# Performance work log

Measured on AMD Instinct MI355X. Metric: run time of the kernel, lower is better.

## Reference

```python
import jax, jax.numpy as jnp
import numpy as np

N_NODES = 100000
N_EDGES = 1600000
F_IN = 128
HID = 128
N_CLS = 10
BN_EPS = 1e-5


def setup_inputs() -> dict:
    key = jax.random.key(0)
    ks = jax.random.split(key, 20)
    d = {}
    d['x'] = jax.random.normal(ks[0], (N_NODES, F_IN), dtype=jnp.float32)
    d['edge_index'] = jax.random.randint(ks[1], (2, N_EDGES), 0, N_NODES, dtype=jnp.int64)
    d['edge_weights'] = jax.random.uniform(ks[2], (N_EDGES,), dtype=jnp.float32)
    s1 = 1.0 / np.sqrt(F_IN)
    s2 = 1.0 / np.sqrt(HID)
    d['W1'] = jax.random.normal(ks[3], (F_IN, HID), dtype=jnp.float32) * s1
    d['b1'] = jax.random.normal(ks[4], (HID,), dtype=jnp.float32) * 0.01
    d['g1'] = jax.random.uniform(ks[5], (HID,), dtype=jnp.float32) + 0.5
    d['be1'] = jax.random.normal(ks[6], (HID,), dtype=jnp.float32) * 0.01
    d['W2'] = jax.random.normal(ks[7], (HID, HID), dtype=jnp.float32) * s2
    d['b2'] = jax.random.normal(ks[8], (HID,), dtype=jnp.float32) * 0.01
    d['g2'] = jax.random.uniform(ks[9], (HID,), dtype=jnp.float32) + 0.5
    d['be2'] = jax.random.normal(ks[10], (HID,), dtype=jnp.float32) * 0.01
    d['W3'] = jax.random.normal(ks[11], (HID, HID), dtype=jnp.float32) * s2
    d['b3'] = jax.random.normal(ks[12], (HID,), dtype=jnp.float32) * 0.01
    d['g3'] = jax.random.uniform(ks[13], (HID,), dtype=jnp.float32) + 0.5
    d['be3'] = jax.random.normal(ks[14], (HID,), dtype=jnp.float32) * 0.01
    d['Wlin'] = jax.random.normal(ks[15], (3 * HID, N_CLS), dtype=jnp.float32) / np.sqrt(3 * HID)
    d['blin'] = jax.random.normal(ks[16], (N_CLS,), dtype=jnp.float32) * 0.01
    return d


def _gcn_norm(edge_index, edge_weights, n):
    # add self loops with weight 1 (PyG gcn_norm default fill_value=1)
    loops = jnp.arange(n, dtype=edge_index.dtype)
    row = jnp.concatenate([edge_index[0], loops])   # source j
    col = jnp.concatenate([edge_index[1], loops])   # target i
    ew = jnp.concatenate([edge_weights, jnp.ones((n,), edge_weights.dtype)])
    deg = jax.ops.segment_sum(ew, col, num_segments=n)  # in-degree by weight
    dis = jnp.where(deg > 0, jax.lax.rsqrt(deg), 0.0)
    norm = dis[row] * ew * dis[col]                     # [E+N]
    return row, col, norm


def _gcn_conv(x, row, col, norm, W, b, n):
    h = x @ W                                            # [N, H]
    msg = h[row] * norm[:, None]                         # gather + scale
    out = jax.ops.segment_sum(msg, col, num_segments=n)  # scatter-add
    return out + b


def _bn_relu(x, g, be):
    # BatchNorm with track_running_stats=False: batch stats, biased variance
    mean = jnp.mean(x, axis=0)
    var = jnp.mean((x - mean) ** 2, axis=0)
    y = (x - mean) * jax.lax.rsqrt(var + BN_EPS) * g + be
    return jax.nn.relu(y)


def reference(x, edge_index, edge_weights, W1, b1, g1, be1, W2, b2, g2, be2,
              W3, b3, g3, be3, Wlin, blin):
    n = x.shape[0]
    row, col, norm = _gcn_norm(edge_index, edge_weights, n)
    o1 = _bn_relu(_gcn_conv(x, row, col, norm, W1, b1, n), g1, be1)
    o2 = _bn_relu(_gcn_conv(o1, row, col, norm, W2, b2, n), g2, be2)
    o3 = _bn_relu(_gcn_conv(o2, row, col, norm, W3, b3, n), g3, be3)
    emb = jnp.concatenate([o1, o2, o3], axis=1)          # [N, 3H]
    return emb @ Wlin + blin                             # [N, C]
```

## Files before the change

kernel.cpp:

```cpp
#include <hip/hip_runtime.h>

#define BN_EPS 1e-5f
#define AGG_GRID 2048
#define RED1 64
#define NB 512
#define CAP 4864
#define BIN_KE 16

typedef __attribute__((ext_vector_type(8))) short short8;
typedef __attribute__((ext_vector_type(4))) float f32x4;

static __device__ __forceinline__ float4 ld4(const float* p){ return *reinterpret_cast<const float4*>(p); }
static __device__ __forceinline__ void st4(float* p, float4 v){ *reinterpret_cast<float4*>(p) = v; }
static __device__ __forceinline__ unsigned short f2bf(float f){
  unsigned u = __float_as_uint(f);
  u += 0x7fffu + ((u>>16)&1u);
  return (unsigned short)(u>>16);
}
static __device__ __forceinline__ void fma_bf4(float4& a, float s, uint2 w){
  float v0 = __uint_as_float(w.x << 16);
  float v1 = __uint_as_float(w.x & 0xffff0000u);
  float v2 = __uint_as_float(w.y << 16);
  float v3 = __uint_as_float(w.y & 0xffff0000u);
  a.x = fmaf(s,v0,a.x); a.y = fmaf(s,v1,a.y); a.z = fmaf(s,v2,a.z); a.w = fmaf(s,v3,a.w);
}
static __device__ __forceinline__ float4 unpack_bf4(uint2 w){
  return make_float4(__uint_as_float(w.x << 16), __uint_as_float(w.x & 0xffff0000u),
                     __uint_as_float(w.y << 16), __uint_as_float(w.y & 0xffff0000u));
}
static __device__ __forceinline__ uint2 pack_bf4(float4 v){
  uint2 pk;
  pk.x = (unsigned)f2bf(v.x) | ((unsigned)f2bf(v.y)<<16);
  pk.y = (unsigned)f2bf(v.z) | ((unsigned)f2bf(v.w)<<16);
  return pk;
}

__global__ __launch_bounds__(256) void k_zero(int* p, int n){
  int i = blockIdx.x*256 + threadIdx.x;
  if (i < n) p[i] = 0;
}

__global__ __launch_bounds__(256) void k_prepW(const float* __restrict__ W, unsigned short* __restrict__ Wt){
  int idx = blockIdx.x*256 + threadIdx.x;
  int k = idx >> 7, n = idx & 127;
  Wt[n*128 + k] = f2bf(W[idx]);
}

__global__ __launch_bounds__(256) void k_prepWlin(const float* __restrict__ Wlin, unsigned short* __restrict__ WlinT){
  int idx = blockIdx.x*256 + threadIdx.x;
  if (idx >= 6144) return;
  int l = idx >> 11, rem = idx & 2047;
  int n = rem >> 7, k = rem & 127;
  float v = (n < 10) ? Wlin[((size_t)l*128 + k)*10 + n] : 0.f;
  WlinT[(size_t)l*2048 + n*128 + k] = f2bf(v);
}

__global__ __launch_bounds__(256) void k_bin(const int* __restrict__ row, const int* __restrict__ col,
                                             const float* __restrict__ ew, int* __restrict__ bucketCnt,
                                             int2* __restrict__ bin, int E){
  __shared__ int hist[NB];
  int t = threadIdx.x;
  hist[t] = 0; hist[t+256] = 0;
  __syncthreads();
  int base0 = blockIdx.x*(256*BIN_KE) + t;
  int rank[BIN_KE];
  #pragma unroll
  for (int j=0;j<BIN_KE;++j){
    int e = base0 + j*256;
    if (e < E) rank[j] = atomicAdd(&hist[col[e]>>8], 1);
  }
  __syncthreads();
  int c0 = hist[t], c1 = hist[t+256];
  __syncthreads();
  if (c0) hist[t]     = atomicAdd(&bucketCnt[t],     c0);
  if (c1) hist[t+256] = atomicAdd(&bucketCnt[t+256], c1);
  __syncthreads();
  #pragma unroll
  for (int j=0;j<BIN_KE;++j){
    int e = base0 + j*256;
    if (e < E){
      int d = col[e];
      int bk = d >> 8;
      int pos = hist[bk] + rank[j];
      if (pos < CAP)
        bin[(size_t)bk*CAP + pos] = make_int2(row[e] | ((d & 255) << 17), __float_as_int(ew[e]));
    }
  }
}

__global__ void k_scan512(const int* __restrict__ cnt, int* __restrict__ start){
  __shared__ int sh[NB];
  int t = threadIdx.x;
  int c = cnt[t]; if (c > CAP) c = CAP;
  sh[t] = c;
  __syncthreads();
  for (int off=1; off<NB; off<<=1){
    int x = (t>=off) ? sh[t-off] : 0;
    __syncthreads();
    sh[t] += x;
    __syncthreads();
  }
  start[t] = sh[t] - c;
}

__global__ __launch_bounds__(256) void k_csr(const int2* __restrict__ bin, const int* __restrict__ bucketCnt,
                                             const int* __restrict__ bucketStart, int2* __restrict__ csr,
                                             int* __restrict__ rstart, float* __restrict__ deg, int N){
  __shared__ int hist[256], scn[256];
  __shared__ float degl[256];
  int b = blockIdx.x, t = threadIdx.x;
  hist[t] = 0; degl[t] = 0.f;
  __syncthreads();
  int m = bucketCnt[b]; if (m > CAP) m = CAP;
  const int2* bb = bin + (size_t)b*CAP;
  for (int i = t; i < m; i += 256){
    int2 r = bb[i];
    int dl = (r.x >> 17) & 255;
    atomicAdd(&hist[dl], 1);
    atomicAdd(&degl[dl], __int_as_float(r.y));
  }
  __syncthreads();
  int c = hist[t];
  scn[t] = c;
  __syncthreads();
  for (int off=1; off<256; off<<=1){
    int x = (t>=off) ? scn[t-off] : 0;
    __syncthreads();
    scn[t] += x;
    __syncthreads();
  }
  int base = bucketStart[b];
  int g = (b<<8) + t;
  if (g < N){
    rstart[g] = base + scn[t] - c;
    deg[g] = 1.f + degl[t];
    if (g == N-1) rstart[N] = base + scn[t];
  }
  __syncthreads();
  hist[t] = scn[t] - c;
  __syncthreads();
  for (int i = t; i < m; i += 256){
    int2 r = bb[i];
    int dl = (r.x >> 17) & 255;
    int pos = atomicAdd(&hist[dl], 1);
    csr[base + pos] = make_int2(r.x & 0x1FFFF, r.y);
  }
}

__global__ __launch_bounds__(256) void k_dis(const float* __restrict__ deg, float* __restrict__ dis, int N){
  int i = blockIdx.x*256 + threadIdx.x;
  if (i < N) dis[i] = rsqrtf(deg[i]);
}

__global__ __launch_bounds__(256) void k_norm(int2* __restrict__ csr, const float* __restrict__ dis, int M){
  int e = blockIdx.x*256 + threadIdx.x;
  if (e < M){
    int2 r = csr[e];
    r.y = __float_as_int(__int_as_float(r.y) * dis[r.x]);
    csr[e] = r;
  }
}

template<bool BN, bool LIN, bool LININIT>
__global__ __launch_bounds__(256) void k_gemm_mfma(const void* __restrict__ Ap, const unsigned short* __restrict__ Wt,
                                                   const float* __restrict__ abv, unsigned short* __restrict__ h,
                                                   const unsigned short* __restrict__ WlinT,
                                                   const float* __restrict__ blin, float* __restrict__ out, int N){
  __shared__ unsigned short Al[64*136];
  __shared__ unsigned short Wl[128*136];
  int t = threadIdx.x;
  int row0 = blockIdx.x*64;
  #pragma unroll
  for (int i=0;i<8;++i){
    int idx = t + 256*i;
    int r = idx>>5, cg = idx&31;
    float4 v;
    if (!BN){
      v = make_float4(0.f,0.f,0.f,0.f);
      if (row0 + r < N) v = ld4((const float*)Ap + ((size_t)(row0+r)<<7) + cg*4);
    } else {
      uint2 raw = make_uint2(0u,0u);
      if (row0 + r < N) raw = *reinterpret_cast<const uint2*>((const unsigned short*)Ap + ((size_t)(row0+r)<<7) + cg*4);
      v = unpack_bf4(raw);
      float4 av = ld4(abv + cg*4), cv = ld4(abv + 128 + cg*4);
      v.x = fmaxf(fmaf(v.x,av.x,cv.x),0.f);
      v.y = fmaxf(fmaf(v.y,av.y,cv.y),0.f);
      v.z = fmaxf(fmaf(v.z,av.z,cv.z),0.f);
      v.w = fmaxf(fmaf(v.w,av.w,cv.w),0.f);
    }
    *reinterpret_cast<uint2*>(&Al[r*136 + cg*4]) = pack_bf4(v);
  }
  #pragma unroll
  for (int i=0;i<8;++i){
    int idx = t + 256*i;
    int n = idx>>4, c8 = idx&15;
    *reinterpret_cast<uint4*>(&Wl[n*136 + c8*8]) =
      *reinterpret_cast<const uint4*>(&Wt[n*128 + c8*8]);
  }

  int w = t>>6, lane = t&63, quad = lane>>4, lr = lane&15;
  short8 bl[4];
  if (LIN){
    #pragma unroll
    for (int q4=0;q4<4;++q4)
      bl[q4] = *reinterpret_cast<const short8*>(&WlinT[lr*128 + q4*32 + quad*8]);
  }
  __syncthreads();

  f32x4 acc[8];
  #pragma unroll
  for (int j=0;j<8;++j) acc[j] = (f32x4){0.f,0.f,0.f,0.f};
  f32x4 accL = (f32x4){0.f,0.f,0.f,0.f};
  #pragma unroll
  for (int kk=0; kk<128; kk+=32){
    short8 a = *reinterpret_cast<const short8*>(&Al[(w*16+lr)*136 + kk + quad*8]);
    #pragma unroll
    for (int j=0;j<8;++j){
      short8 b = *reinterpret_cast<const short8*>(&Wl[(j*16+lr)*136 + kk + quad*8]);
      acc[j] = __builtin_amdgcn_mfma_f32_16x16x32_bf16(a, b, acc[j], 0, 0, 0);
    }
    if (LIN) accL = __builtin_amdgcn_mfma_f32_16x16x32_bf16(a, bl[kk>>5], accL, 0, 0, 0);
  }
  if (LIN && lr < 10){
    #pragma unroll
    for (int r=0;r<4;++r){
      int rr = row0 + w*16 + quad*4 + r;
      if (rr < N){
        if (LININIT) out[(size_t)rr*10 + lr] = blin[lr] + accL[r];
        else         out[(size_t)rr*10 + lr] += accL[r];
      }
    }
  }
  __syncthreads();
  #pragma unroll
  for (int j=0;j<8;++j)
    #pragma unroll
    for (int r=0;r<4;++r)
      Al[(w*16 + quad*4 + r)*136 + j*16 + lr] = f2bf(acc[j][r]);
  __syncthreads();
  #pragma unroll
  for (int i=0;i<8;++i){
    int idx = t + 256*i;
    int r = idx>>5, cg = idx&31;
    if (row0 + r < N)
      *reinterpret_cast<uint2*>(&h[((size_t)(row0+r)<<7) + cg*4]) =
        *reinterpret_cast<const uint2*>(&Al[r*136 + cg*4]);
  }
}

__global__ __launch_bounds__(256) void k_agg(const unsigned short* __restrict__ h, const int2* __restrict__ csr,
                                             const int* __restrict__ rstart, const float* __restrict__ dis,
                                             const float* __restrict__ bias, unsigned short* __restrict__ o,
                                             float* __restrict__ partials, int N){
  __shared__ float ls[256];
  int t = threadIdx.x;
  ls[t] = 0.f;
  __syncthreads();
  int lane = t & 31, gy = t >> 5;
  float4 bv = ld4(bias + lane*4);
  float4 ssum = make_float4(0.f,0.f,0.f,0.f);
  float4 ssq  = make_float4(0.f,0.f,0.f,0.f);
  for (int g = blockIdx.x*8 + gy; g < N; g += AGG_GRID*8){
    int s = rstart[g], n = rstart[g+1] - s;
    float dg = dis[g];
    float4 acc = make_float4(0.f,0.f,0.f,0.f);
    fma_bf4(acc, dg*dg, *reinterpret_cast<const uint2*>(h + ((size_t)g<<7) + lane*4));
    int i = 0;
    for (; i+3 < n; i += 4){
      int2 e0 = csr[s+i], e1 = csr[s+i+1], e2 = csr[s+i+2], e3 = csr[s+i+3];
      uint2 r0 = *reinterpret_cast<const uint2*>(h + ((size_t)e0.x<<7) + lane*4);
      uint2 r1 = *reinterpret_cast<const uint2*>(h + ((size_t)e1.x<<7) + lane*4);
      uint2 r2 = *reinterpret_cast<const uint2*>(h + ((size_t)e2.x<<7) + lane*4);
      uint2 r3 = *reinterpret_cast<const uint2*>(h + ((size_t)e3.x<<7) + lane*4);
      fma_bf4(acc, __int_as_float(e0.y)*dg, r0);
      fma_bf4(acc, __int_as_float(e1.y)*dg, r1);
      fma_bf4(acc, __int_as_float(e2.y)*dg, r2);
      fma_bf4(acc, __int_as_float(e3.y)*dg, r3);
    }
    for (; i < n; ++i){
      int2 e0 = csr[s+i];
      fma_bf4(acc, __int_as_float(e0.y)*dg, *reinterpret_cast<const uint2*>(h + ((size_t)e0.x<<7) + lane*4));
    }
    acc.x += bv.x; acc.y += bv.y; acc.z += bv.z; acc.w += bv.w;
    *reinterpret_cast<uint2*>(o + ((size_t)g<<7) + lane*4) = pack_bf4(acc);
    ssum.x += acc.x; ssum.y += acc.y; ssum.z += acc.z; ssum.w += acc.w;
    ssq.x = fmaf(acc.x,acc.x,ssq.x); ssq.y = fmaf(acc.y,acc.y,ssq.y);
    ssq.z = fmaf(acc.z,acc.z,ssq.z); ssq.w = fmaf(acc.w,acc.w,ssq.w);
  }
  int f = lane*4;
  atomicAdd(&ls[f+0], ssum.x); atomicAdd(&ls[f+1], ssum.y);
  atomicAdd(&ls[f+2], ssum.z); atomicAdd(&ls[f+3], ssum.w);
  atomicAdd(&ls[128+f+0], ssq.x); atomicAdd(&ls[128+f+1], ssq.y);
  atomicAdd(&ls[128+f+2], ssq.z); atomicAdd(&ls[128+f+3], ssq.w);
  __syncthreads();
  partials[(size_t)blockIdx.x*256 + t] = ls[t];
}

__global__ __launch_bounds__(256) void k_bn_red1(const float* __restrict__ partials, float* __restrict__ out1){
  int t = threadIdx.x, b = blockIdx.x;
  int rows = AGG_GRID / RED1;
  const float* p = partials + (size_t)b*rows*256;
  float s0 = 0.f, s1 = 0.f, s2 = 0.f, s3 = 0.f;
  for (int i=0;i<rows;i+=4){
    s0 += p[(size_t)(i+0)*256 + t];
    s1 += p[(size_t)(i+1)*256 + t];
    s2 += p[(size_t)(i+2)*256 + t];
    s3 += p[(size_t)(i+3)*256 + t];
  }
  out1[(size_t)b*256 + t] = (s0+s1)+(s2+s3);
}

__global__ void k_bn_fin(const float* __restrict__ out1, const float* __restrict__ gam,
                         const float* __restrict__ bet, float* __restrict__ ab, int N){
  __shared__ float sh[256];
  int t = threadIdx.x;
  float s = 0.f;
  #pragma unroll 4
  for (int i=0;i<RED1;++i) s += out1[(size_t)i*256 + t];
  sh[t] = s;
  __syncthreads();
  if (t < 128){
    float invN = 1.f/(float)N;
    float mean = sh[t]*invN;
    float var = fmaxf(sh[128+t]*invN - mean*mean, 0.f);
    float a = gam[t]*rsqrtf(var + BN_EPS);
    ab[t] = a;
    ab[128+t] = bet[t] - mean*a;
  }
}

__global__ __launch_bounds__(256) void k_lin(const unsigned short* __restrict__ o, const float* __restrict__ Wl_g,
                                             const float* __restrict__ ab, float* __restrict__ out, int N){
  __shared__ float Wl[1280];
  __shared__ float abL[256];
  int t = threadIdx.x;
  for (int i=t;i<1280;i+=256) Wl[i] = Wl_g[i];
  abL[t] = ab[t];
  __syncthreads();
  int row = blockIdx.x*256 + t;
  if (row >= N) return;
  float acc[10];
  #pragma unroll
  for (int c=0;c<10;++c) acc[c] = out[(size_t)row*10 + c];
  const unsigned short* orow = o + ((size_t)row<<7);
  #pragma unroll 4
  for (int k=0;k<128;k+=4){
    float4 v = unpack_bf4(*reinterpret_cast<const uint2*>(orow + k));
    float4 av = ld4(abL + k), cv = ld4(abL + 128 + k);
    v.x = fmaxf(fmaf(v.x,av.x,cv.x),0.f);
    v.y = fmaxf(fmaf(v.y,av.y,cv.y),0.f);
    v.z = fmaxf(fmaf(v.z,av.z,cv.z),0.f);
    v.w = fmaxf(fmaf(v.w,av.w,cv.w),0.f);
    #pragma unroll
    for (int c=0;c<10;++c){
      acc[c] = fmaf(v.x, Wl[(k+0)*10+c], acc[c]);
      acc[c] = fmaf(v.y, Wl[(k+1)*10+c], acc[c]);
      acc[c] = fmaf(v.z, Wl[(k+2)*10+c], acc[c]);
      acc[c] = fmaf(v.w, Wl[(k+3)*10+c], acc[c]);
    }
  }
  #pragma unroll
  for (int c=0;c<10;++c) out[(size_t)row*10 + c] = acc[c];
}


extern "C" void kernel_launch(void* const* d_in, const int* in_sizes, int n_in,
                              void* d_out, int out_size, void* d_ws, size_t ws_size,
                              hipStream_t stream){
  const float* x    = (const float*)d_in[0];
  const int*   ei   = (const int*)d_in[1];
  const float* ew   = (const float*)d_in[2];
  const float* W[3]  = {(const float*)d_in[3], (const float*)d_in[7],  (const float*)d_in[11]};
  const float* b[3]  = {(const float*)d_in[4], (const float*)d_in[8],  (const float*)d_in[12]};
  const float* g[3]  = {(const float*)d_in[5], (const float*)d_in[9],  (const float*)d_in[13]};
  const float* be[3] = {(const float*)d_in[6], (const float*)d_in[10], (const float*)d_in[14]};
  const float* Wlin = (const float*)d_in[15];
  const float* blin = (const float*)d_in[16];
  float* out = (float*)d_out;

  int N = in_sizes[0] / 128;
  int E = in_sizes[2];
  const int* row = ei;
  const int* col = ei + E;

  char* p = (char*)d_ws;
  auto carve = [&](size_t bytes) -> void* {
    void* q = (void*)p;
    p += (bytes + 255) & ~(size_t)255;
    return q;
  };
  int*   bucketCnt   = (int*)  carve((size_t)NB*4);
  int*   bucketStart = (int*)  carve((size_t)NB*4);
  float* deg      = (float*)carve((size_t)N*4);
  float* dis      = (float*)carve((size_t)N*4);
  int*   rstart   = (int*)  carve((size_t)(N+1)*4);
  float* partials = (float*)carve((size_t)AGG_GRID*256*4);
  float* red1     = (float*)carve((size_t)RED1*256*4);
  float* ab       = (float*)carve(3*256*4);
  unsigned short* Wt    = (unsigned short*)carve((size_t)3*128*128*2);
  unsigned short* WlinT = (unsigned short*)carve((size_t)3*16*128*2);
  unsigned short* h  = (unsigned short*)carve((size_t)N*128*2);
  unsigned short* o  = (unsigned short*)carve((size_t)N*128*2);
  int2*  csr      = (int2*) carve((size_t)E*8);
  int2*  bin      = (int2*) carve((size_t)NB*CAP*8);

  int gN = (N+255)/256, gE = (E+255)/256;
  int gBin = (E + 256*BIN_KE - 1) / (256*BIN_KE);

  k_zero<<<2,256,0,stream>>>(bucketCnt, NB);
  for (int l=0;l<3;++l)
    k_prepW<<<64,256,0,stream>>>(W[l], Wt + (size_t)l*128*128);
  k_prepWlin<<<24,256,0,stream>>>(Wlin, WlinT);
  k_bin    <<<gBin,256,0,stream>>>(row, col, ew, bucketCnt, bin, E);
  k_scan512<<<1,NB,0,stream>>>(bucketCnt, bucketStart);
  k_csr    <<<NB,256,0,stream>>>(bin, bucketCnt, bucketStart, csr, rstart, deg, N);
  k_dis    <<<gN,256,0,stream>>>(deg, dis, N);
  k_norm   <<<gE,256,0,stream>>>(csr, dis, E);

  int gGemm = (N+63)/64;
  k_gemm_mfma<false,false,false><<<gGemm,256,0,stream>>>(x, Wt, nullptr, h, nullptr, nullptr, nullptr, N);
  k_agg    <<<AGG_GRID,256,0,stream>>>(h, csr, rstart, dis, b[0], o, partials, N);
  k_bn_red1<<<RED1,256,0,stream>>>(partials, red1);
  k_bn_fin <<<1,256,0,stream>>>(red1, g[0], be[0], ab, N);
  k_gemm_mfma<true,true,true><<<gGemm,256,0,stream>>>(o, Wt + 128*128, ab, h, WlinT, blin, out, N);
  k_agg    <<<AGG_GRID,256,0,stream>>>(h, csr, rstart, dis, b[1], o, partials, N);
  k_bn_red1<<<RED1,256,0,stream>>>(partials, red1);
  k_bn_fin <<<1,256,0,stream>>>(red1, g[1], be[1], ab + 256, N);
  k_gemm_mfma<true,true,false><<<gGemm,256,0,stream>>>(o, Wt + 2*128*128, ab + 256, h, WlinT + 2048, blin, out, N);
  k_agg    <<<AGG_GRID,256,0,stream>>>(h, csr, rstart, dis, b[2], o, partials, N);
  k_bn_red1<<<RED1,256,0,stream>>>(partials, red1);
  k_bn_fin <<<1,256,0,stream>>>(red1, g[2], be[2], ab + 512, N);
  k_lin    <<<gN,256,0,stream>>>(o, Wlin + (size_t)2*1280, ab + 512, out, N);
}
```

Before: 515.5 us.

## Fold source-degree scaling into GEMM epilogue and fuse BN reduction into aggregation

The source-side D^-1/2 factor moves out of the per-edge weights and into the GEMM epilogue, which scales each h row by dis[row]. The target-side factor is applied once per node at the end of aggregation. This removes the k_norm and k_dis passes over edges and nodes. The BatchNorm statistics reduction is folded into k_agg with a last-block-done atomic counter, replacing two extra kernels per layer, and the weight prep and zeroing kernels are merged into one launch. In exchange, a single block serially reduces all 2048 partials, and h is now stored in bf16 after scaling by dis, which slightly changes rounding.

```diff
diff --git a/kernel.cpp b/kernel.cpp
--- a/kernel.cpp
+++ b/kernel.cpp
@@ -2,7 +2,6 @@
 
 #define BN_EPS 1e-5f
 #define AGG_GRID 2048
-#define RED1 64
 #define NB 512
 #define CAP 4864
 #define BIN_KE 16
@@ -11,7 +10,6 @@
 typedef __attribute__((ext_vector_type(4))) float f32x4;
 
 static __device__ __forceinline__ float4 ld4(const float* p){ return *reinterpret_cast<const float4*>(p); }
-static __device__ __forceinline__ void st4(float* p, float4 v){ *reinterpret_cast<float4*>(p) = v; }
 static __device__ __forceinline__ unsigned short f2bf(float f){
   unsigned u = __float_as_uint(f);
   u += 0x7fffu + ((u>>16)&1u);
@@ -35,24 +33,27 @@
   return pk;
 }
 
-__global__ __launch_bounds__(256) void k_zero(int* p, int n){
-  int i = blockIdx.x*256 + threadIdx.x;
-  if (i < n) p[i] = 0;
-}
-
-__global__ __launch_bounds__(256) void k_prepW(const float* __restrict__ W, unsigned short* __restrict__ Wt){
+__global__ __launch_bounds__(256) void k_prep(const float* __restrict__ W0, const float* __restrict__ W1,
+                                              const float* __restrict__ W2, const float* __restrict__ Wlin,
+                                              unsigned short* __restrict__ Wt, unsigned short* __restrict__ WlinT,
+                                              int* __restrict__ bucketCnt, int* __restrict__ counters){
   int idx = blockIdx.x*256 + threadIdx.x;
-  int k = idx >> 7, n = idx & 127;
-  Wt[n*128 + k] = f2bf(W[idx]);
-}
-
-__global__ __launch_bounds__(256) void k_prepWlin(const float* __restrict__ Wlin, unsigned short* __restrict__ WlinT){
-  int idx = blockIdx.x*256 + threadIdx.x;
-  if (idx >= 6144) return;
-  int l = idx >> 11, rem = idx & 2047;
-  int n = rem >> 7, k = rem & 127;
-  float v = (n < 10) ? Wlin[((size_t)l*128 + k)*10 + n] : 0.f;
-  WlinT[(size_t)l*2048 + n*128 + k] = f2bf(v);
+  if (idx < NB) bucketCnt[idx] = 0;
+  else if (idx < NB + 8) counters[idx - NB] = 0;
+  int widx = idx - 1024;
+  if (widx >= 0 && widx < 49152){
+    int l = widx >> 14, rem = widx & 16383;
+    int k = rem >> 7, n = rem & 127;
+    const float* W = (l==0) ? W0 : ((l==1) ? W1 : W2);
+    Wt[(size_t)l*16384 + n*128 + k] = f2bf(W[rem]);
+  }
+  int lidx = widx - 49152;
+  if (lidx >= 0 && lidx < 6144){
+    int l = lidx >> 11, rem = lidx & 2047;
+    int n = rem >> 7, k = rem & 127;
+    float v = (n < 10) ? Wlin[((size_t)l*128 + k)*10 + n] : 0.f;
+    WlinT[(size_t)l*2048 + n*128 + k] = f2bf(v);
+  }
 }
 
 __global__ __launch_bounds__(256) void k_bin(const int* __restrict__ row, const int* __restrict__ col,
@@ -105,7 +106,7 @@
 
 __global__ __launch_bounds__(256) void k_csr(const int2* __restrict__ bin, const int* __restrict__ bucketCnt,
                                              const int* __restrict__ bucketStart, int2* __restrict__ csr,
-                                             int* __restrict__ rstart, float* __restrict__ deg, int N){
+                                             int* __restrict__ rstart, float* __restrict__ dis, int N){
   __shared__ int hist[256], scn[256];
   __shared__ float degl[256];
   int b = blockIdx.x, t = threadIdx.x;
@@ -133,7 +134,7 @@
   int g = (b<<8) + t;
   if (g < N){
     rstart[g] = base + scn[t] - c;
-    deg[g] = 1.f + degl[t];
+    dis[g] = rsqrtf(1.f + degl[t]);
     if (g == N-1) rstart[N] = base + scn[t];
   }
   __syncthreads();
@@ -147,23 +148,10 @@
   }
 }
 
-__global__ __launch_bounds__(256) void k_dis(const float* __restrict__ deg, float* __restrict__ dis, int N){
-  int i = blockIdx.x*256 + threadIdx.x;
-  if (i < N) dis[i] = rsqrtf(deg[i]);
-}
-
-__global__ __launch_bounds__(256) void k_norm(int2* __restrict__ csr, const float* __restrict__ dis, int M){
-  int e = blockIdx.x*256 + threadIdx.x;
-  if (e < M){
-    int2 r = csr[e];
-    r.y = __float_as_int(__int_as_float(r.y) * dis[r.x]);
-    csr[e] = r;
-  }
-}
-
 template<bool BN, bool LIN, bool LININIT>
 __global__ __launch_bounds__(256) void k_gemm_mfma(const void* __restrict__ Ap, const unsigned short* __restrict__ Wt,
-                                                   const float* __restrict__ abv, unsigned short* __restrict__ h,
+                                                   const float* __restrict__ abv, const float* __restrict__ dis,
+                                                   unsigned short* __restrict__ h,
                                                    const unsigned short* __restrict__ WlinT,
                                                    const float* __restrict__ blin, float* __restrict__ out, int N){
   __shared__ unsigned short Al[64*136];
@@ -231,12 +219,18 @@
       }
     }
   }
+  float drow[4];
+  #pragma unroll
+  for (int r=0;r<4;++r){
+    int rr = row0 + w*16 + quad*4 + r;
+    drow[r] = (rr < N) ? dis[rr] : 0.f;
+  }
   __syncthreads();
   #pragma unroll
   for (int j=0;j<8;++j)
     #pragma unroll
     for (int r=0;r<4;++r)
-      Al[(w*16 + quad*4 + r)*136 + j*16 + lr] = f2bf(acc[j][r]);
+      Al[(w*16 + quad*4 + r)*136 + j*16 + lr] = f2bf(acc[j][r] * drow[r]);
   __syncthreads();
   #pragma unroll
   for (int i=0;i<8;++i){
@@ -251,8 +245,11 @@
 __global__ __launch_bounds__(256) void k_agg(const unsigned short* __restrict__ h, const int2* __restrict__ csr,
                                              const int* __restrict__ rstart, const float* __restrict__ dis,
                                              const float* __restrict__ bias, unsigned short* __restrict__ o,
-                                             float* __restrict__ partials, int N){
+                                             float* __restrict__ partials, int* __restrict__ counter,
+                                             const float* __restrict__ gam, const float* __restrict__ bet,
+                                             float* __restrict__ ab, int N){
   __shared__ float ls[256];
+  __shared__ int isLast;
   int t = threadIdx.x;
   ls[t] = 0.f;
   __syncthreads();
@@ -263,8 +260,7 @@
   for (int g = blockIdx.x*8 + gy; g < N; g += AGG_GRID*8){
     int s = rstart[g], n = rstart[g+1] - s;
     float dg = dis[g];
-    float4 acc = make_float4(0.f,0.f,0.f,0.f);
-    fma_bf4(acc, dg*dg, *reinterpret_cast<const uint2*>(h + ((size_t)g<<7) + lane*4));
+    float4 acc = unpack_bf4(*reinterpret_cast<const uint2*>(h + ((size_t)g<<7) + lane*4));
     int i = 0;
     for (; i+3 < n; i += 4){
       int2 e0 = csr[s+i], e1 = csr[s+i+1], e2 = csr[s+i+2], e3 = csr[s+i+3];
@@ -272,16 +268,17 @@
       uint2 r1 = *reinterpret_cast<const uint2*>(h + ((size_t)e1.x<<7) + lane*4);
       uint2 r2 = *reinterpret_cast<const uint2*>(h + ((size_t)e2.x<<7) + lane*4);
       uint2 r3 = *reinterpret_cast<const uint2*>(h + ((size_t)e3.x<<7) + lane*4);
-      fma_bf4(acc, __int_as_float(e0.y)*dg, r0);
-      fma_bf4(acc, __int_as_float(e1.y)*dg, r1);
-      fma_bf4(acc, __int_as_float(e2.y)*dg, r2);
-      fma_bf4(acc, __int_as_float(e3.y)*dg, r3);
+      fma_bf4(acc, __int_as_float(e0.y), r0);
+      fma_bf4(acc, __int_as_float(e1.y), r1);
+      fma_bf4(acc, __int_as_float(e2.y), r2);
+      fma_bf4(acc, __int_as_float(e3.y), r3);
     }
     for (; i < n; ++i){
       int2 e0 = csr[s+i];
-      fma_bf4(acc, __int_as_float(e0.y)*dg, *reinterpret_cast<const uint2*>(h + ((size_t)e0.x<<7) + lane*4));
-    }
-    acc.x += bv.x; acc.y += bv.y; acc.z += bv.z; acc.w += bv.w;
+      fma_bf4(acc, __int_as_float(e0.y), *reinterpret_cast<const uint2*>(h + ((size_t)e0.x<<7) + lane*4));
+    }
+    acc.x = fmaf(acc.x, dg, bv.x); acc.y = fmaf(acc.y, dg, bv.y);
+    acc.z = fmaf(acc.z, dg, bv.z); acc.w = fmaf(acc.w, dg, bv.w);
     *reinterpret_cast<uint2*>(o + ((size_t)g<<7) + lane*4) = pack_bf4(acc);
     ssum.x += acc.x; ssum.y += acc.y; ssum.z += acc.z; ssum.w += acc.w;
     ssq.x = fmaf(acc.x,acc.x,ssq.x); ssq.y = fmaf(acc.y,acc.y,ssq.y);
@@ -294,35 +291,25 @@
   atomicAdd(&ls[128+f+2], ssq.z); atomicAdd(&ls[128+f+3], ssq.w);
   __syncthreads();
   partials[(size_t)blockIdx.x*256 + t] = ls[t];
-}
-
-__global__ __launch_bounds__(256) void k_bn_red1(const float* __restrict__ partials, float* __restrict__ out1){
-  int t = threadIdx.x, b = blockIdx.x;
-  int rows = AGG_GRID / RED1;
-  const float* p = partials + (size_t)b*rows*256;
+  __threadfence();
+  __syncthreads();
+  if (t == 0) isLast = (atomicAdd(counter, 1) == AGG_GRID - 1);
+  __syncthreads();
+  if (!isLast) return;
+  __threadfence();
   float s0 = 0.f, s1 = 0.f, s2 = 0.f, s3 = 0.f;
-  for (int i=0;i<rows;i+=4){
-    s0 += p[(size_t)(i+0)*256 + t];
-    s1 += p[(size_t)(i+1)*256 + t];
-    s2 += p[(size_t)(i+2)*256 + t];
-    s3 += p[(size_t)(i+3)*256 + t];
-  }
-  out1[(size_t)b*256 + t] = (s0+s1)+(s2+s3);
-}
-
-__global__ void k_bn_fin(const float* __restrict__ out1, const float* __restrict__ gam,
-                         const float* __restrict__ bet, float* __restrict__ ab, int N){
-  __shared__ float sh[256];
-  int t = threadIdx.x;
-  float s = 0.f;
-  #pragma unroll 4
-  for (int i=0;i<RED1;++i) s += out1[(size_t)i*256 + t];
-  sh[t] = s;
+  for (int i=0;i<AGG_GRID;i+=4){
+    s0 += partials[(size_t)(i+0)*256 + t];
+    s1 += partials[(size_t)(i+1)*256 + t];
+    s2 += partials[(size_t)(i+2)*256 + t];
+    s3 += partials[(size_t)(i+3)*256 + t];
+  }
+  ls[t] = (s0+s1)+(s2+s3);
   __syncthreads();
   if (t < 128){
     float invN = 1.f/(float)N;
-    float mean = sh[t]*invN;
-    float var = fmaxf(sh[128+t]*invN - mean*mean, 0.f);
+    float mean = ls[t]*invN;
+    float var = fmaxf(ls[128+t]*invN - mean*mean, 0.f);
     float a = gam[t]*rsqrtf(var + BN_EPS);
     ab[t] = a;
     ab[128+t] = bet[t] - mean*a;
@@ -391,11 +378,10 @@
   };
   int*   bucketCnt   = (int*)  carve((size_t)NB*4);
   int*   bucketStart = (int*)  carve((size_t)NB*4);
-  float* deg      = (float*)carve((size_t)N*4);
+  int*   counters    = (int*)  carve(8*4);
   float* dis      = (float*)carve((size_t)N*4);
   int*   rstart   = (int*)  carve((size_t)(N+1)*4);
   float* partials = (float*)carve((size_t)AGG_GRID*256*4);
-  float* red1     = (float*)carve((size_t)RED1*256*4);
   float* ab       = (float*)carve(3*256*4);
   unsigned short* Wt    = (unsigned short*)carve((size_t)3*128*128*2);
   unsigned short* WlinT = (unsigned short*)carve((size_t)3*16*128*2);
@@ -404,31 +390,20 @@
   int2*  csr      = (int2*) carve((size_t)E*8);
   int2*  bin      = (int2*) carve((size_t)NB*CAP*8);
 
-  int gN = (N+255)/256, gE = (E+255)/256;
+  int gN = (N+255)/256;
   int gBin = (E + 256*BIN_KE - 1) / (256*BIN_KE);
 
-  k_zero<<<2,256,0,stream>>>(bucketCnt, NB);
-  for (int l=0;l<3;++l)
-    k_prepW<<<64,256,0,stream>>>(W[l], Wt + (size_t)l*128*128);
-  k_prepWlin<<<24,256,0,stream>>>(Wlin, WlinT);
+  k_prep   <<<221,256,0,stream>>>(W[0], W[1], W[2], Wlin, Wt, WlinT, bucketCnt, counters);
   k_bin    <<<gBin,256,0,stream>>>(row, col, ew, bucketCnt, bin, E);
   k_scan512<<<1,NB,0,stream>>>(bucketCnt, bucketStart);
-  k_csr    <<<NB,256,0,stream>>>(bin, bucketCnt, bucketStart, csr, rstart, deg, N);
-  k_dis    <<<gN,256,0,stream>>>(deg, dis, N);
-  k_norm   <<<gE,256,0,stream>>>(csr, dis, E);
+  k_csr    <<<NB,256,0,stream>>>(bin, bucketCnt, bucketStart, csr, rstart, dis, N);
 
   int gGemm = (N+63)/64;
-  k_gemm_mfma<false,false,false><<<gGemm,256,0,stream>>>(x, Wt, nullptr, h, nullptr, nullptr, nullptr, N);
-  k_agg    <<<AGG_GRID,256,0,stream>>>(h, csr, rstart, dis, b[0], o, partials, N);
-  k_bn_red1<<<RED1,256,0,stream>>>(partials, red1);
-  k_bn_fin <<<1,256,0,stream>>>(red1, g[0], be[0], ab, N);
-  k_gemm_mfma<true,true,true><<<gGemm,256,0,stream>>>(o, Wt + 128*128, ab, h, WlinT, blin, out, N);
-  k_agg    <<<AGG_GRID,256,0,stream>>>(h, csr, rstart, dis, b[1], o, partials, N);
-  k_bn_red1<<<RED1,256,0,stream>>>(partials, red1);
-  k_bn_fin <<<1,256,0,stream>>>(red1, g[1], be[1], ab + 256, N);
-  k_gemm_mfma<true,true,false><<<gGemm,256,0,stream>>>(o, Wt + 2*128*128, ab + 256, h, WlinT + 2048, blin, out, N);
-  k_agg    <<<AGG_GRID,256,0,stream>>>(h, csr, rstart, dis, b[2], o, partials, N);
-  k_bn_red1<<<RED1,256,0,stream>>>(partials, red1);
-  k_bn_fin <<<1,256,0,stream>>>(red1, g[2], be[2], ab + 512, N);
-  k_lin    <<<gN,256,0,stream>>>(o, Wlin + (size_t)2*1280, ab + 512, out, N);
-}
+  k_gemm_mfma<false,false,false><<<gGemm,256,0,stream>>>(x, Wt, nullptr, dis, h, nullptr, nullptr, nullptr, N);
+  k_agg<<<AGG_GRID,256,0,stream>>>(h, csr, rstart, dis, b[0], o, partials, counters+0, g[0], be[0], ab, N);
+  k_gemm_mfma<true,true,true><<<gGemm,256,0,stream>>>(o, Wt + 16384, ab, dis, h, WlinT, blin, out, N);
+  k_agg<<<AGG_GRID,256,0,stream>>>(h, csr, rstart, dis, b[1], o, partials, counters+1, g[1], be[1], ab + 256, N);
+  k_gemm_mfma<true,true,false><<<gGemm,256,0,stream>>>(o, Wt + 32768, ab + 256, dis, h, WlinT + 2048, blin, out, N);
+  k_agg<<<AGG_GRID,256,0,stream>>>(h, csr, rstart, dis, b[2], o, partials, counters+2, g[2], be[2], ab + 512, N);
+  k_lin<<<gN,256,0,stream>>>(o, Wlin + (size_t)2*1280, ab + 512, out, N);
+}
```

New measurement: 1.083 ms. +110.0%, slower.
